# Kernel optimization log

Hardware: AMD Instinct MI355X
Metric: run time of the kernel (lower is better)

## Reference

```python
import jax, jax.numpy as jnp
import numpy as np

COS_EPS = 1e-8   # torch F.cosine_similarity norm clamp
LOG_EPS = 1e-12  # log stabilizer in Sinkhorn
SINK_ITERS = 5
SINK_EPS = 0.5


def _pairwise_cosine(x1, x2):
    # x1, x2: [b, c, hw]; cosine similarity between all channel pairs along hw
    n1 = x1 / jnp.maximum(jnp.linalg.norm(x1, axis=-1, keepdims=True), COS_EPS)
    n2 = x2 / jnp.maximum(jnp.linalg.norm(x2, axis=-1, keepdims=True), COS_EPS)
    return jnp.einsum('bik,bjk->bij', n1, n2)  # [b, c, c]


def _M(C, u, v, eps):
    # C: [b,c,c]; u, v: [b,c,hw]. With b==c==hw this broadcasts to [b,c,hw,hw],
    # exactly mirroring the torch broadcast in the original module.
    return (-C + u[..., None] + v[..., None, :]) / eps


def _sinkhorn(p1, p2, C, iters=SINK_ITERS, eps=SINK_EPS):
    u = jnp.zeros_like(p1)
    v = jnp.zeros_like(p2)
    for _ in range(iters):
        # Gauss-Seidel: v-update uses the freshly updated u (as in the original loop)
        u = eps * (jnp.log(p1 + LOG_EPS)
                   - jax.scipy.special.logsumexp(_M(C, u, v, eps), axis=-1)) + u
        v = eps * (jnp.log(p2 + LOG_EPS)
                   - jax.scipy.special.logsumexp(
                       jnp.swapaxes(_M(C, u, v, eps), -2, -1), axis=-1)) + v
    pi = jnp.exp(_M(C, u, v, eps))
    return jnp.mean(jnp.sum(pi * C, axis=(-2, -1)))


def _emd_single(x1, x2):
    b, c, h, w = x1.shape
    x1 = x1.reshape(b, c, h * w)
    x2 = x2.reshape(b, c, h * w)
    p1 = jax.nn.softmax(x1, axis=-1)  # [b, c, hw]
    p2 = jax.nn.softmax(x2, axis=-1)
    C = 1.0 - _pairwise_cosine(x1, x2)  # [b, c, c]
    Cmin = jnp.min(C, axis=-1, keepdims=True)
    Cmax = jnp.max(C, axis=-1, keepdims=True)
    C = (C - Cmin) / (Cmax - Cmin)
    return _sinkhorn(p1, p2, C)


def setup_inputs() -> dict:
    key = jax.random.key(0)
    k1, k2, k3, k4 = jax.random.split(key, 4)
    B, C, H, W = 64, 64, 8, 8  # requires B == C == H*W (see original broadcast)
    shp = (B, C, H, W)
    return {
        'f1_0': jax.random.normal(k1, shp, dtype=jnp.float32),
        'f1_1': jax.random.normal(k2, shp, dtype=jnp.float32),
        'f2_0': jax.random.normal(k3, shp, dtype=jnp.float32),
        'f2_1': jax.random.normal(k4, shp, dtype=jnp.float32),
    }


def reference(f1_0, f1_1, f2_0, f2_1):
    loss = _emd_single(f1_0, f2_0) + _emd_single(f1_1, f2_1)
    return loss / 2.0
```

## Files before the change

kernel.cpp:

```cpp
#include <hip/hip_runtime.h>
#include <math.h>


#define SINK_ITERS 5
#define LOGEPS 1e-12f
#define COSEPS 1e-8f

typedef __attribute__((ext_vector_type(8))) short bf16x8;
typedef __attribute__((ext_vector_type(4))) float f32x4;

__device__ __forceinline__ float wave_sum(float v) {
    #pragma unroll
    for (int o = 32; o; o >>= 1) v += __shfl_xor(v, o);
    return v;
}
__device__ __forceinline__ float wave_max(float v) {
    #pragma unroll
    for (int o = 32; o; o >>= 1) v = fmaxf(v, __shfl_xor(v, o));
    return v;
}
__device__ __forceinline__ float fast_rcp(float v) {
    return __builtin_amdgcn_rcpf(v);
}
__device__ __forceinline__ unsigned short f2bf(float f) {
    unsigned int u = __float_as_uint(f);
    u = (u + 0x7FFFu + ((u >> 16) & 1u)) >> 16;
    return (unsigned short)u;
}
__device__ __forceinline__ float bf2f(unsigned short h) {
    return __uint_as_float(((unsigned int)h) << 16);
}
__device__ __forceinline__ int frag_idx(int k, int n) {
    return ((k >> 5) << 9) + (((((k & 31) >> 3) << 4) | n) << 3) + (k & 7);
}
__device__ __forceinline__ void split8(const float* f, bf16x8& hi, bf16x8& lo) {
    #pragma unroll
    for (int j = 0; j < 8; j++) {
        unsigned short h = f2bf(f[j]);
        hi[j] = (short)h;
        lo[j] = (short)f2bf(f[j] - bf2f(h));
    }
}

__global__ __launch_bounds__(256, 2) void emd_fused(
        const float* __restrict__ f10, const float* __restrict__ f11,
        const float* __restrict__ f20, const float* __restrict__ f21,
        float* __restrict__ out)
{
    __shared__ float Ksh[64][68];
    __shared__ float KTsh[64][68];
    __shared__ float Csh[64][68];
    __shared__ float p1sh[64][17];
    __shared__ float p2sh[64][17];
    __shared__ __align__(16) short aF[1024];
    __shared__ __align__(16) short bF[1024];
    __shared__ float wsum[4];

    const int tid = threadIdx.x, w = tid >> 6, lane = tid & 63;
    const int g = blockIdx.x, c = blockIdx.y, p = blockIdx.z;
    const float* x1 = p ? f11 : f10;
    const float* x2 = p ? f21 : f20;

    const int b0 = (g << 4) | (w << 2);
    #pragma unroll
    for (int qq = 0; qq < 4; qq++) {
        const int rowoff = (((b0 + qq) << 6) | c) << 6;
        float xv1 = x1[rowoff + lane];
        float e1 = __expf(xv1 - wave_max(xv1));
        p1sh[lane][(w << 2) + qq] = e1 * fast_rcp(wave_sum(e1)) + LOGEPS;
        float xv2 = x2[rowoff + lane];
        float e2 = __expf(xv2 - wave_max(xv2));
        p2sh[lane][(w << 2) + qq] = e2 * fast_rcp(wave_sum(e2)) + LOGEPS;
    }
    if (tid < 128) {
        bf16x8 one;
        #pragma unroll
        for (int j = 0; j < 8; j++) one[j] = (short)0x3F80;
        *(bf16x8*)&bF[((tid >> 6) << 9) + ((tid & 63) << 3)] = one;
    }

    const int base = c << 12;
    const float4* x1g = (const float4*)(x1 + base);
    #pragma unroll
    for (int m = 0; m < 4; m++) {
        int idx = tid + (m << 8);
        float4 v = x1g[idx];
        int r = idx >> 4, k0 = (idx & 15) << 2;
        Ksh[r][k0] = v.x; Ksh[r][k0 + 1] = v.y;
        Ksh[r][k0 + 2] = v.z; Ksh[r][k0 + 3] = v.w;
    }

    float x2r[64];
    const float4* x2g = (const float4*)(x2 + base + (lane << 6));
    float ss2 = 0.f;
    #pragma unroll
    for (int k4 = 0; k4 < 16; k4++) {
        float4 v = x2g[k4];
        x2r[4 * k4] = v.x; x2r[4 * k4 + 1] = v.y;
        x2r[4 * k4 + 2] = v.z; x2r[4 * k4 + 3] = v.w;
        ss2 += v.x * v.x + v.y * v.y + v.z * v.z + v.w * v.w;
    }
    const float i2 = 1.0f / fmaxf(sqrtf(ss2), COSEPS);
    __syncthreads();

    __shared__ float inv1[64];
    if (tid < 64) {
        const float4* xr = (const float4*)(&Ksh[tid][0]);
        float s = 0.f;
        #pragma unroll
        for (int k4 = 0; k4 < 16; k4++) {
            float4 v = xr[k4];
            s += v.x * v.x + v.y * v.y + v.z * v.z + v.w * v.w;
        }
        inv1[tid] = 1.0f / fmaxf(sqrtf(s), COSEPS);
    }
    __syncthreads();

    float kvr[16];
    #pragma unroll
    for (int m = 0; m < 16; m++) {
        const int i = (m << 2) | w;
        const float4* xr = (const float4*)(&Ksh[i][0]);
        float acc = 0.f;
        #pragma unroll
        for (int k4 = 0; k4 < 16; k4++) {
            float4 xv = xr[k4];
            acc = fmaf(xv.x, x2r[4 * k4], acc);
            acc = fmaf(xv.y, x2r[4 * k4 + 1], acc);
            acc = fmaf(xv.z, x2r[4 * k4 + 2], acc);
            acc = fmaf(xv.w, x2r[4 * k4 + 3], acc);
        }
        float cv = 1.0f - acc * inv1[i] * i2;
        float mn = cv, mx = cv;
        #pragma unroll
        for (int o = 32; o; o >>= 1) {
            mn = fminf(mn, __shfl_xor(mn, o));
            mx = fmaxf(mx, __shfl_xor(mx, o));
        }
        cv = (cv - mn) / (mx - mn);
        Csh[i][lane] = cv;
        float kv = __expf(-2.0f * cv);
        KTsh[lane][i] = kv;
        kvr[m] = kv;
    }
    __syncthreads();
    #pragma unroll
    for (int m = 0; m < 16; m++) Ksh[(m << 2) | w][lane] = kvr[m];
    __syncthreads();

    const int q = lane >> 4, n = lane & 15;
    const int am = (w << 4) | n;
    bf16x8 KhiF[2], KloF[2], KThiF[2], KTloF[2], KChiF[2], KCloF[2];
    #pragma unroll
    for (int ks = 0; ks < 2; ks++) {
        const int k0 = (ks << 5) + (q << 3);
        float fk[8], fkt[8], fkc[8];
        #pragma unroll
        for (int j = 0; j < 8; j++) {
            fk[j]  = Ksh[am][k0 + j];
            fkt[j] = KTsh[am][k0 + j];
            fkc[j] = fk[j] * Csh[am][k0 + j];
        }
        split8(fk,  KhiF[ks],  KloF[ks]);
        split8(fkt, KThiF[ks], KTloF[ks]);
        split8(fkc, KChiF[ks], KCloF[ks]);
    }
    float p1r[4], p2r[4], a[4];
    #pragma unroll
    for (int reg = 0; reg < 4; reg++) {
        const int row = (w << 4) + (q << 2) + reg;
        p1r[reg] = p1sh[row][n];
        p2r[reg] = p2sh[row][n];
    }
    __syncthreads();

    #pragma unroll 1
    for (int it = 0; it < SINK_ITERS; it++) {
        bf16x8 bf0 = *(const bf16x8*)&bF[lane << 3];
        bf16x8 bf1 = *(const bf16x8*)&bF[512 + (lane << 3)];
        f32x4 acc = {0.f, 0.f, 0.f, 0.f};
        acc = __builtin_amdgcn_mfma_f32_16x16x32_bf16(KhiF[0], bf0, acc, 0, 0, 0);
        acc = __builtin_amdgcn_mfma_f32_16x16x32_bf16(KhiF[1], bf1, acc, 0, 0, 0);
        acc = __builtin_amdgcn_mfma_f32_16x16x32_bf16(KloF[0], bf0, acc, 0, 0, 0);
        acc = __builtin_amdgcn_mfma_f32_16x16x32_bf16(KloF[1], bf1, acc, 0, 0, 0);
        #pragma unroll
        for (int reg = 0; reg < 4; reg++) {
            a[reg] = p1r[reg] * fast_rcp(acc[reg]);
            aF[frag_idx((w << 4) + (q << 2) + reg, n)] = (short)f2bf(a[reg]);
        }
        __syncthreads();

        bf16x8 af0 = *(const bf16x8*)&aF[lane << 3];
        bf16x8 af1 = *(const bf16x8*)&aF[512 + (lane << 3)];
        f32x4 acc2 = {0.f, 0.f, 0.f, 0.f};
        acc2 = __builtin_amdgcn_mfma_f32_16x16x32_bf16(KThiF[0], af0, acc2, 0, 0, 0);
        acc2 = __builtin_amdgcn_mfma_f32_16x16x32_bf16(KThiF[1], af1, acc2, 0, 0, 0);
        acc2 = __builtin_amdgcn_mfma_f32_16x16x32_bf16(KTloF[0], af0, acc2, 0, 0, 0);
        acc2 = __builtin_amdgcn_mfma_f32_16x16x32_bf16(KTloF[1], af1, acc2, 0, 0, 0);
        #pragma unroll
        for (int reg = 0; reg < 4; reg++) {
            float bnew = p2r[reg] * fast_rcp(acc2[reg]);
            bF[frag_idx((w << 4) + (q << 2) + reg, n)] = (short)f2bf(bnew);
        }
        __syncthreads();
    }

    {
        bf16x8 bf0 = *(const bf16x8*)&bF[lane << 3];
        bf16x8 bf1 = *(const bf16x8*)&bF[512 + (lane << 3)];
        f32x4 acc3 = {0.f, 0.f, 0.f, 0.f};
        acc3 = __builtin_amdgcn_mfma_f32_16x16x32_bf16(KChiF[0], bf0, acc3, 0, 0, 0);
        acc3 = __builtin_amdgcn_mfma_f32_16x16x32_bf16(KChiF[1], bf1, acc3, 0, 0, 0);
        acc3 = __builtin_amdgcn_mfma_f32_16x16x32_bf16(KCloF[0], bf0, acc3, 0, 0, 0);
        acc3 = __builtin_amdgcn_mfma_f32_16x16x32_bf16(KCloF[1], bf1, acc3, 0, 0, 0);
        float part = a[0] * acc3[0] + a[1] * acc3[1] +
                     a[2] * acc3[2] + a[3] * acc3[3];
        float tot = wave_sum(part);
        if (lane == 0) wsum[w] = tot;
    }
    __syncthreads();
    if (tid == 0)
        atomicAdd(out, (wsum[0] + wsum[1] + wsum[2] + wsum[3]) * (1.0f / 8192.0f));
}

extern "C" void kernel_launch(void* const* d_in, const int* in_sizes, int n_in,
                              void* d_out, int out_size, void* d_ws, size_t ws_size,
                              hipStream_t stream) {
    const float* f10 = (const float*)d_in[0];
    const float* f11 = (const float*)d_in[1];
    const float* f20 = (const float*)d_in[2];
    const float* f21 = (const float*)d_in[3];
    float* out = (float*)d_out;

    hipMemsetAsync(out, 0, sizeof(float), stream);
    emd_fused<<<dim3(4, 64, 2), 256, 0, stream>>>(f10, f11, f20, f21, out);
}
```

Baseline: 84.51 us.

## Compute pairwise cosine Gram matrix with split-bf16 MFMA instead of scalar FMAs

Replaces the per-thread scalar 64x64x64 dot-product loop, which held x2 in 64 registers, with a split-bf16 (hi/lo, three-term) MFMA Gram computation. Both inputs are staged in shared memory and the norms are computed in parallel. The min/max normalisation now works on the MFMA output layout using 16-lane shuffles, and the shared-memory fragment loads are vectorised. The intent is to cut VALU work and register pressure in the setup phase, at some cost in precision from the bf16x3 approximation.

```diff
diff --git a/kernel.cpp b/kernel.cpp
--- a/kernel.cpp
+++ b/kernel.cpp
@@ -40,6 +40,11 @@
         hi[j] = (short)h;
         lo[j] = (short)f2bf(f[j] - bf2f(h));
     }
+}
+__device__ __forceinline__ void load8(const float* p, float* f) {
+    float4 a0 = ((const float4*)p)[0], a1 = ((const float4*)p)[1];
+    f[0] = a0.x; f[1] = a0.y; f[2] = a0.z; f[3] = a0.w;
+    f[4] = a1.x; f[5] = a1.y; f[6] = a1.z; f[7] = a1.w;
 }
 
 __global__ __launch_bounds__(256, 2) void emd_fused(
@@ -54,6 +59,7 @@
     __shared__ float p2sh[64][17];
     __shared__ __align__(16) short aF[1024];
     __shared__ __align__(16) short bF[1024];
+    __shared__ float inv1[64], inv2[64];
     __shared__ float wsum[4];
 
     const int tid = threadIdx.x, w = tid >> 6, lane = tid & 63;
@@ -81,86 +87,98 @@
 
     const int base = c << 12;
     const float4* x1g = (const float4*)(x1 + base);
+    const float4* x2g = (const float4*)(x2 + base);
     #pragma unroll
     for (int m = 0; m < 4; m++) {
         int idx = tid + (m << 8);
-        float4 v = x1g[idx];
         int r = idx >> 4, k0 = (idx & 15) << 2;
-        Ksh[r][k0] = v.x; Ksh[r][k0 + 1] = v.y;
-        Ksh[r][k0 + 2] = v.z; Ksh[r][k0 + 3] = v.w;
-    }
-
-    float x2r[64];
-    const float4* x2g = (const float4*)(x2 + base + (lane << 6));
-    float ss2 = 0.f;
-    #pragma unroll
-    for (int k4 = 0; k4 < 16; k4++) {
-        float4 v = x2g[k4];
-        x2r[4 * k4] = v.x; x2r[4 * k4 + 1] = v.y;
-        x2r[4 * k4 + 2] = v.z; x2r[4 * k4 + 3] = v.w;
-        ss2 += v.x * v.x + v.y * v.y + v.z * v.z + v.w * v.w;
-    }
-    const float i2 = 1.0f / fmaxf(sqrtf(ss2), COSEPS);
-    __syncthreads();
-
-    __shared__ float inv1[64];
-    if (tid < 64) {
-        const float4* xr = (const float4*)(&Ksh[tid][0]);
+        *(float4*)&Ksh[r][k0] = x1g[idx];
+        *(float4*)&Csh[r][k0] = x2g[idx];
+    }
+    __syncthreads();
+
+    if (tid < 128) {
+        int r = tid & 63;
+        const float4* xr = (const float4*)((tid < 64) ? &Ksh[r][0] : &Csh[r][0]);
         float s = 0.f;
         #pragma unroll
         for (int k4 = 0; k4 < 16; k4++) {
             float4 v = xr[k4];
             s += v.x * v.x + v.y * v.y + v.z * v.z + v.w * v.w;
         }
-        inv1[tid] = 1.0f / fmaxf(sqrtf(s), COSEPS);
-    }
-    __syncthreads();
-
-    float kvr[16];
-    #pragma unroll
-    for (int m = 0; m < 16; m++) {
-        const int i = (m << 2) | w;
-        const float4* xr = (const float4*)(&Ksh[i][0]);
-        float acc = 0.f;
-        #pragma unroll
-        for (int k4 = 0; k4 < 16; k4++) {
-            float4 xv = xr[k4];
-            acc = fmaf(xv.x, x2r[4 * k4], acc);
-            acc = fmaf(xv.y, x2r[4 * k4 + 1], acc);
-            acc = fmaf(xv.z, x2r[4 * k4 + 2], acc);
-            acc = fmaf(xv.w, x2r[4 * k4 + 3], acc);
-        }
-        float cv = 1.0f - acc * inv1[i] * i2;
-        float mn = cv, mx = cv;
-        #pragma unroll
-        for (int o = 32; o; o >>= 1) {
+        float inv = 1.0f / fmaxf(sqrtf(s), COSEPS);
+        if (tid < 64) inv1[r] = inv; else inv2[r] = inv;
+    }
+    __syncthreads();
+
+    const int q = lane >> 4, n = lane & 15;
+    const int arow = (w << 4) | n;
+    bf16x8 Ahi[2], Alo[2];
+    #pragma unroll
+    for (int ks = 0; ks < 2; ks++) {
+        float fa[8];
+        load8(&Ksh[arow][(ks << 5) + (q << 3)], fa);
+        split8(fa, Ahi[ks], Alo[ks]);
+    }
+    f32x4 accT[4];
+    #pragma unroll
+    for (int jt = 0; jt < 4; jt++) {
+        bf16x8 Bhi[2], Blo[2];
+        #pragma unroll
+        for (int ks = 0; ks < 2; ks++) {
+            float fb[8];
+            load8(&Csh[(jt << 4) | n][(ks << 5) + (q << 3)], fb);
+            split8(fb, Bhi[ks], Blo[ks]);
+        }
+        f32x4 gacc = {0.f, 0.f, 0.f, 0.f};
+        gacc = __builtin_amdgcn_mfma_f32_16x16x32_bf16(Ahi[0], Bhi[0], gacc, 0, 0, 0);
+        gacc = __builtin_amdgcn_mfma_f32_16x16x32_bf16(Ahi[1], Bhi[1], gacc, 0, 0, 0);
+        gacc = __builtin_amdgcn_mfma_f32_16x16x32_bf16(Ahi[0], Blo[0], gacc, 0, 0, 0);
+        gacc = __builtin_amdgcn_mfma_f32_16x16x32_bf16(Ahi[1], Blo[1], gacc, 0, 0, 0);
+        gacc = __builtin_amdgcn_mfma_f32_16x16x32_bf16(Alo[0], Bhi[0], gacc, 0, 0, 0);
+        gacc = __builtin_amdgcn_mfma_f32_16x16x32_bf16(Alo[1], Bhi[1], gacc, 0, 0, 0);
+        accT[jt] = gacc;
+    }
+    __syncthreads();
+
+    #pragma unroll
+    for (int reg = 0; reg < 4; reg++) {
+        const int i = (w << 4) + (q << 2) + reg;
+        const float i1v = inv1[i];
+        float cv[4];
+        #pragma unroll
+        for (int jt = 0; jt < 4; jt++)
+            cv[jt] = 1.0f - accT[jt][reg] * i1v * inv2[(jt << 4) | n];
+        float mn = fminf(fminf(cv[0], cv[1]), fminf(cv[2], cv[3]));
+        float mx = fmaxf(fmaxf(cv[0], cv[1]), fmaxf(cv[2], cv[3]));
+        #pragma unroll
+        for (int o = 1; o < 16; o <<= 1) {
             mn = fminf(mn, __shfl_xor(mn, o));
             mx = fmaxf(mx, __shfl_xor(mx, o));
         }
-        cv = (cv - mn) / (mx - mn);
-        Csh[i][lane] = cv;
-        float kv = __expf(-2.0f * cv);
-        KTsh[lane][i] = kv;
-        kvr[m] = kv;
-    }
-    __syncthreads();
-    #pragma unroll
-    for (int m = 0; m < 16; m++) Ksh[(m << 2) | w][lane] = kvr[m];
-    __syncthreads();
-
-    const int q = lane >> 4, n = lane & 15;
-    const int am = (w << 4) | n;
+        const float irange = fast_rcp(mx - mn);
+        #pragma unroll
+        for (int jt = 0; jt < 4; jt++) {
+            const int j = (jt << 4) | n;
+            float cnorm = (cv[jt] - mn) * irange;
+            float kv = __expf(-2.0f * cnorm);
+            Csh[i][j] = cnorm;
+            Ksh[i][j] = kv;
+            KTsh[j][i] = kv;
+        }
+    }
+    __syncthreads();
+
     bf16x8 KhiF[2], KloF[2], KThiF[2], KTloF[2], KChiF[2], KCloF[2];
     #pragma unroll
     for (int ks = 0; ks < 2; ks++) {
         const int k0 = (ks << 5) + (q << 3);
         float fk[8], fkt[8], fkc[8];
-        #pragma unroll
-        for (int j = 0; j < 8; j++) {
-            fk[j]  = Ksh[am][k0 + j];
-            fkt[j] = KTsh[am][k0 + j];
-            fkc[j] = fk[j] * Csh[am][k0 + j];
-        }
+        load8(&Ksh[arow][k0], fk);
+        load8(&KTsh[arow][k0], fkt);
+        load8(&Csh[arow][k0], fkc);
+        #pragma unroll
+        for (int j = 0; j < 8; j++) fkc[j] *= fk[j];
         split8(fk,  KhiF[ks],  KloF[ks]);
         split8(fkt, KThiF[ks], KTloF[ks]);
         split8(fkc, KChiF[ks], KCloF[ks]);
```

New measurement: 77.80 us. 1.09x faster.
